# Optimization experiments

Hardware: AMD Instinct MI355X
Metric: run time of the kernel (lower is better)

The kernel has to match this reference:

```python
import jax, jax.numpy as jnp
import numpy as np

# Config constants (match init_kwargs)
THR = 0.2
TEMPERATURE = 0.1
BORDER_RM = 2
H0C, W0C = 60, 80  # L = 4800
H1C, W1C = 60, 80  # S = 4800


def setup_inputs() -> dict:
    key = jax.random.key(0)
    k0, k1 = jax.random.split(key)
    feat_c0 = jax.random.normal(k0, (2, 4800, 256), dtype=jnp.float32)
    feat_c1 = jax.random.normal(k1, (2, 4800, 256), dtype=jnp.float32)
    return {"feat_c0": feat_c0, "feat_c1": feat_c1}


def _border_mask_1d(h, w, b):
    """Flattened [h*w] bool mask that is False within b of any border."""
    ih = jnp.arange(h)
    iw = jnp.arange(w)
    mh = (ih >= b) & (ih < h - b)
    mw = (iw >= b) & (iw < w - b)
    return (mh[:, None] & mw[None, :]).reshape(-1)


def reference(feat_c0, feat_c1):
    N, L, C = feat_c0.shape
    # Normalize features and compute similarity (dual-softmax)
    scale = 1.0 / (C ** 0.5)
    sim = jnp.einsum('nlc,nsc->nls', feat_c0 * scale, feat_c1 * scale) / TEMPERATURE
    conf = jax.nn.softmax(sim, axis=1) * jax.nn.softmax(sim, axis=2)  # [N, L, S]

    # Threshold + border removal (mask_border path, no padding masks)
    bm0 = _border_mask_1d(H0C, W0C, BORDER_RM)  # [L]
    bm1 = _border_mask_1d(H1C, W1C, BORDER_RM)  # [S]
    mask = (conf > THR) & bm0[None, :, None] & bm1[None, None, :]

    # Mutual nearest neighbor
    mask = mask \
        & (conf == jnp.max(conf, axis=2, keepdims=True)) \
        & (conf == jnp.max(conf, axis=1, keepdims=True))

    # Per-row match: j index of the (at most one) surviving entry, and its conf.
    # Fixed-shape analogue of torch.where extraction: mconf==0 means no match.
    mask_v = jnp.any(mask, axis=2)                         # [N, L]
    j_ids = jnp.argmax(mask, axis=2)                       # [N, L]
    mconf = jnp.take_along_axis(conf, j_ids[..., None], axis=2)[..., 0]
    mconf = jnp.where(mask_v, mconf, 0.0)                  # [N, L]

    return conf, mask_v, j_ids, mconf
```

## Files before the change

### kernel.cpp

```cpp
#include <hip/hip_runtime.h>
#include <hip/hip_bf16.h>
#include <cstdint>

#define L_DIM 4800
#define C_DIM 256
#define CONF_ELEMS ((size_t)2 * L_DIM * L_DIM)

typedef _Float16 f16x8 __attribute__((ext_vector_type(8)));
typedef float f32x4 __attribute__((ext_vector_type(4)));

typedef const __attribute__((address_space(1))) uint32_t glb_u32;
typedef __attribute__((address_space(3))) uint32_t lds_u32;

#define WS_F16_NEEDED 15705600

__global__ __launch_bounds__(256) void k_cvt2(const float* __restrict__ f0,
                                              const float* __restrict__ f1,
                                              _Float16* __restrict__ h0,
                                              _Float16* __restrict__ h1) {
    int b = blockIdx.x;
    const float* src = (b < 1200) ? f0 : f1;
    _Float16* dst = (b < 1200) ? h0 : h1;
    int i = (b < 1200 ? b : b - 1200) * 256 + threadIdx.x;
    const float4* s4 = (const float4*)src;
    float4 a = s4[(size_t)i * 2], c = s4[(size_t)i * 2 + 1];
    f16x8 h = { (_Float16)a.x, (_Float16)a.y, (_Float16)a.z, (_Float16)a.w,
                (_Float16)c.x, (_Float16)c.y, (_Float16)c.z, (_Float16)c.w };
    *(f16x8*)(dst + (size_t)i * 8) = h;
}

__global__ __launch_bounds__(256) void k_reduceA(const float* __restrict__ partA,
                                                 float* __restrict__ invsum) {
    int i = blockIdx.x * 256 + threadIdx.x;
    if (i >= 19200) return;
    int base = (i < 9600) ? 0 : 50;
    int j = (i < 9600) ? i : i - 9600;
    float s = 0.f;
#pragma unroll 10
    for (int k = 0; k < 50; ++k)
        s += partA[(size_t)(base + k) * 9600 + j];
    invsum[i] = 1.0f / s;
}

template<bool F16SRC, bool FINAL>
__global__ __launch_bounds__(256) void k_gemm2(const void* __restrict__ srcA,
                                               const void* __restrict__ srcB,
                                               float* __restrict__ conf,
                                               const float* __restrict__ invsum,
                                               float* __restrict__ partA,
                                               unsigned long long* __restrict__ rowbest,
                                               unsigned* __restrict__ colbest) {
    const int xcd = blockIdx.x & 7;
    const int idx = blockIdx.x >> 3;
    const int t   = xcd * 625 + idx;
    const int n   = t / 2500;
    const int rem = t - n * 2500;
    const int ty  = rem / 50;
    const int tx  = rem - ty * 50;
    const int l0  = ty * 96;
    const int s0  = tx * 96;

    __shared__ __align__(16) _Float16 As[96 * 64];
    __shared__ __align__(16) _Float16 Bs[96 * 64];
    __shared__ __align__(16) char redbuf[2304];

    const int tid  = threadIdx.x;
    const int lane = tid & 63;
    const int w    = tid >> 6;
    const int wr   = w >> 1, wc = w & 1;
    const int q    = lane >> 4, r16 = lane & 15;

    f32x4 acc[3][3] = {};

    const _Float16* Ah = (const _Float16*)srcA + ((size_t)n * L_DIM + l0) * C_DIM;
    const _Float16* Bh = (const _Float16*)srcB + ((size_t)n * L_DIM + s0) * C_DIM;
    const float*    Af = (const float*)srcA + ((size_t)n * L_DIM + l0) * C_DIM;
    const float*    Bf = (const float*)srcB + ((size_t)n * L_DIM + s0) * C_DIM;

    for (int kt = 0; kt < 4; ++kt) {
        const int k0 = kt * 64;
        __syncthreads();
        if constexpr (F16SRC) {
#pragma unroll
            for (int i = 0; i < 3; ++i) {
                int c   = tid + i * 256;
                int row = c >> 3;
                int kc  = (c & 7) ^ (row & 7);
                __builtin_amdgcn_global_load_lds(
                    (glb_u32*)(Ah + (size_t)row * C_DIM + k0 + kc * 8),
                    (lds_u32*)(As + (i * 256 + w * 64) * 8), 16, 0, 0);
                __builtin_amdgcn_global_load_lds(
                    (glb_u32*)(Bh + (size_t)row * C_DIM + k0 + kc * 8),
                    (lds_u32*)(Bs + (i * 256 + w * 64) * 8), 16, 0, 0);
            }
        } else {
#pragma unroll
            for (int i = 0; i < 3; ++i) {
                int c   = tid + i * 256;
                int row = c >> 3;
                int kc  = (c & 7) ^ (row & 7);
                const float* pa = Af + (size_t)row * C_DIM + k0 + kc * 8;
                const float* pb = Bf + (size_t)row * C_DIM + k0 + kc * 8;
                float4 a0 = ((const float4*)pa)[0], a1 = ((const float4*)pa)[1];
                float4 b0 = ((const float4*)pb)[0], b1 = ((const float4*)pb)[1];
                f16x8 ha = { (_Float16)a0.x, (_Float16)a0.y, (_Float16)a0.z, (_Float16)a0.w,
                             (_Float16)a1.x, (_Float16)a1.y, (_Float16)a1.z, (_Float16)a1.w };
                f16x8 hb = { (_Float16)b0.x, (_Float16)b0.y, (_Float16)b0.z, (_Float16)b0.w,
                             (_Float16)b1.x, (_Float16)b1.y, (_Float16)b1.z, (_Float16)b1.w };
                *(f16x8*)(As + (size_t)c * 8) = ha;
                *(f16x8*)(Bs + (size_t)c * 8) = hb;
            }
        }
        __syncthreads();

        f16x8 af[2][3], bf[2][3];
#pragma unroll
        for (int m = 0; m < 3; ++m) {
            int row = wr * 48 + m * 16 + r16;
#pragma unroll
            for (int ks = 0; ks < 2; ++ks)
                af[ks][m] = *(const f16x8*)(As + row * 64 + (((ks * 4 + q) ^ (row & 7)) * 8));
        }
#pragma unroll
        for (int nn = 0; nn < 3; ++nn) {
            int row = wc * 48 + nn * 16 + r16;
#pragma unroll
            for (int ks = 0; ks < 2; ++ks)
                bf[ks][nn] = *(const f16x8*)(Bs + row * 64 + (((ks * 4 + q) ^ (row & 7)) * 8));
        }
#pragma unroll
        for (int ks = 0; ks < 2; ++ks)
#pragma unroll
            for (int m = 0; m < 3; ++m)
#pragma unroll
                for (int nn = 0; nn < 3; ++nn)
                    acc[m][nn] = __builtin_amdgcn_mfma_f32_16x16x32_f16(af[ks][m], bf[ks][nn], acc[m][nn], 0, 0, 0);
    }

    const float SIM_SCALE = 0.0390625f;

    if constexpr (!FINAL) {
        float* redR = (float*)redbuf;
        float* redC = (float*)(redbuf + 768);
        float cp[3] = {0.f, 0.f, 0.f};
#pragma unroll
        for (int m = 0; m < 3; ++m) {
#pragma unroll
            for (int reg = 0; reg < 4; ++reg) {
                float rsum = 0.f;
#pragma unroll
                for (int nn = 0; nn < 3; ++nn) {
                    float e = __expf(acc[m][nn][reg] * SIM_SCALE);
                    rsum += e;
                    cp[nn] += e;
                }
                rsum += __shfl_xor(rsum, 1);
                rsum += __shfl_xor(rsum, 2);
                rsum += __shfl_xor(rsum, 4);
                rsum += __shfl_xor(rsum, 8);
                if (r16 == 0)
                    redR[wc * 96 + wr * 48 + m * 16 + q * 4 + reg] = rsum;
            }
        }
#pragma unroll
        for (int nn = 0; nn < 3; ++nn) {
            float v = cp[nn];
            v += __shfl_xor(v, 16);
            v += __shfl_xor(v, 32);
            if (q == 0)
                redC[wr * 96 + wc * 48 + nn * 16 + r16] = v;
        }
        __syncthreads();
        if (tid < 96) {
            partA[(size_t)tx * 9600 + n * L_DIM + l0 + tid] = redR[tid] + redR[96 + tid];
        } else if (tid < 192) {
            int c = tid - 96;
            partA[(size_t)(50 + ty) * 9600 + n * L_DIM + s0 + c] = redC[c] + redC[96 + c];
        }
    } else {
        unsigned long long* redRB = (unsigned long long*)redbuf;
        unsigned* redCB = (unsigned*)(redbuf + 1536);
        const size_t base = (size_t)n * L_DIM * L_DIM;
        float ivC[3];
#pragma unroll
        for (int nn = 0; nn < 3; ++nn)
            ivC[nn] = invsum[9600 + n * L_DIM + s0 + wc * 48 + nn * 16 + r16];
        float cmx[3] = {0.f, 0.f, 0.f};
#pragma unroll
        for (int m = 0; m < 3; ++m) {
#pragma unroll
            for (int reg = 0; reg < 4; ++reg) {
                const int grow = l0 + wr * 48 + m * 16 + q * 4 + reg;
                const float ivR = invsum[n * L_DIM + grow];
                const size_t rowoff = base + (size_t)grow * L_DIM;
                float bv = -1.f; int bc = 0;
#pragma unroll
                for (int nn = 0; nn < 3; ++nn) {
                    const int gcol = s0 + wc * 48 + nn * 16 + r16;
                    float cf = __expf(acc[m][nn][reg] * (2.0f * SIM_SCALE)) * ivR * ivC[nn];
                    __builtin_nontemporal_store(cf, &conf[rowoff + gcol]);
                    cmx[nn] = fmaxf(cmx[nn], cf);
                    if (cf > bv) { bv = cf; bc = gcol; }
                }
                unsigned long long pack =
                    ((unsigned long long)__float_as_uint(bv) << 32) |
                    (unsigned long long)(0xFFFFFFFFu - (unsigned)bc);
#pragma unroll
                for (int d = 1; d < 16; d <<= 1) {
                    unsigned long long o = __shfl_xor(pack, d);
                    if (o > pack) pack = o;
                }
                if (r16 == 0)
                    redRB[wc * 96 + wr * 48 + m * 16 + q * 4 + reg] = pack;
            }
        }
#pragma unroll
        for (int nn = 0; nn < 3; ++nn) {
            float v = cmx[nn];
            v = fmaxf(v, __shfl_xor(v, 16));
            v = fmaxf(v, __shfl_xor(v, 32));
            if (q == 0)
                redCB[wr * 96 + wc * 48 + nn * 16 + r16] = __float_as_uint(v);
        }
        __syncthreads();
        if (tid < 96) {
            unsigned long long p0 = redRB[tid], p1 = redRB[96 + tid];
            rowbest[(size_t)tx * 9600 + n * L_DIM + l0 + tid] = (p0 > p1) ? p0 : p1;
        } else if (tid < 192) {
            int c = tid - 96;
            colbest[(size_t)ty * 9600 + n * L_DIM + s0 + c] = max(redCB[c], redCB[96 + c]);
        }
    }
}

__global__ __launch_bounds__(256) void k_match(const unsigned long long* __restrict__ rowbest,
                                               const unsigned* __restrict__ colbest,
                                               float* __restrict__ out) {
    int i = blockIdx.x * 256 + threadIdx.x;
    if (i >= 2 * L_DIM) return;
    unsigned long long p = 0ull;
#pragma unroll 10
    for (int k = 0; k < 50; ++k) {
        unsigned long long o = rowbest[(size_t)k * 9600 + i];
        if (o > p) p = o;
    }
    int n = i / L_DIM, l = i % L_DIM;
    float v = __uint_as_float((unsigned)(p >> 32));
    int cand = (int)(0xFFFFFFFFu - (unsigned)(p & 0xFFFFFFFFull));
    if (cand < 0 || cand >= L_DIM) cand = 0;
    unsigned cmu = 0u;
#pragma unroll 10
    for (int k = 0; k < 50; ++k)
        cmu = max(cmu, colbest[(size_t)k * 9600 + n * L_DIM + cand]);
    int h0 = l / 80, w0 = l % 80;
    int h1 = cand / 80, w1 = cand % 80;
    bool bm0 = (h0 >= 2) && (h0 < 58) && (w0 >= 2) && (w0 < 78);
    bool bm1 = (h1 >= 2) && (h1 < 58) && (w1 >= 2) && (w1 < 78);
    float cm = __uint_as_float(cmu);
    bool mask = (v > 0.2f) && bm0 && bm1 && (v == cm);
    out[CONF_ELEMS + i]         = mask ? 1.0f : 0.0f;
    out[CONF_ELEMS + 9600 + i]  = mask ? (float)cand : 0.0f;
    out[CONF_ELEMS + 19200 + i] = mask ? v : 0.0f;
}

extern "C" void kernel_launch(void* const* d_in, const int* in_sizes, int n_in,
                              void* d_out, int out_size, void* d_ws, size_t ws_size,
                              hipStream_t stream) {
    const float* f0 = (const float*)d_in[0];
    const float* f1 = (const float*)d_in[1];
    float* out = (float*)d_out;

    float* invsum = (float*)d_ws;
    float* partA = (float*)((char*)d_ws + 115200);
    unsigned long long* rowbest = (unsigned long long*)((char*)d_ws + 115200);
    unsigned* colbest = (unsigned*)((char*)d_ws + 3955200);
    _Float16* h0 = (_Float16*)((char*)d_ws + 5875200);
    _Float16* h1 = h0 + (size_t)2 * L_DIM * C_DIM;

    const bool usef16 = ws_size >= WS_F16_NEEDED;

    if (usef16) {
        k_cvt2<<<dim3(2400), 256, 0, stream>>>(f0, f1, h0, h1);
        k_gemm2<true, false><<<dim3(5000), 256, 0, stream>>>(
            h0, h1, out, invsum, partA, rowbest, colbest);
        k_reduceA<<<dim3(75), 256, 0, stream>>>(partA, invsum);
        k_gemm2<true, true><<<dim3(5000), 256, 0, stream>>>(
            h0, h1, out, invsum, partA, rowbest, colbest);
    } else {
        k_gemm2<false, false><<<dim3(5000), 256, 0, stream>>>(
            f0, f1, out, invsum, partA, rowbest, colbest);
        k_reduceA<<<dim3(75), 256, 0, stream>>>(partA, invsum);
        k_gemm2<false, true><<<dim3(5000), 256, 0, stream>>>(
            f0, f1, out, invsum, partA, rowbest, colbest);
    }
    k_match<<<dim3(38), 256, 0, stream>>>(rowbest, colbest, out);
}
```

Baseline: 135.5 us.

## Give each wave private LDS tiles to drop block-wide barriers in GEMM loop

New measurement: 161.4 us. 1.19x slower.

```diff
diff --git a/kernel.cpp b/kernel.cpp
--- a/kernel.cpp
+++ b/kernel.cpp
@@ -60,8 +60,7 @@
     const int l0  = ty * 96;
     const int s0  = tx * 96;
 
-    __shared__ __align__(16) _Float16 As[96 * 64];
-    __shared__ __align__(16) _Float16 Bs[96 * 64];
+    __shared__ __align__(16) _Float16 Sg[4 * 2 * 48 * 64];
     __shared__ __align__(16) char redbuf[2304];
 
     const int tid  = threadIdx.x;
@@ -70,35 +69,41 @@
     const int wr   = w >> 1, wc = w & 1;
     const int q    = lane >> 4, r16 = lane & 15;
 
+    _Float16* myA = Sg + w * 6144;
+    _Float16* myB = myA + 3072;
+
     f32x4 acc[3][3] = {};
 
-    const _Float16* Ah = (const _Float16*)srcA + ((size_t)n * L_DIM + l0) * C_DIM;
-    const _Float16* Bh = (const _Float16*)srcB + ((size_t)n * L_DIM + s0) * C_DIM;
-    const float*    Af = (const float*)srcA + ((size_t)n * L_DIM + l0) * C_DIM;
-    const float*    Bf = (const float*)srcB + ((size_t)n * L_DIM + s0) * C_DIM;
+    const _Float16* Ah = (const _Float16*)srcA + ((size_t)n * L_DIM + l0 + wr * 48) * C_DIM;
+    const _Float16* Bh = (const _Float16*)srcB + ((size_t)n * L_DIM + s0 + wc * 48) * C_DIM;
+    const float*    Af = (const float*)srcA + ((size_t)n * L_DIM + l0 + wr * 48) * C_DIM;
+    const float*    Bf = (const float*)srcB + ((size_t)n * L_DIM + s0 + wc * 48) * C_DIM;
 
     for (int kt = 0; kt < 4; ++kt) {
         const int k0 = kt * 64;
-        __syncthreads();
+        asm volatile("s_waitcnt lgkmcnt(0)" ::: "memory");
+        __builtin_amdgcn_sched_barrier(0);
         if constexpr (F16SRC) {
 #pragma unroll
-            for (int i = 0; i < 3; ++i) {
-                int c   = tid + i * 256;
-                int row = c >> 3;
-                int kc  = (c & 7) ^ (row & 7);
+            for (int jj = 0; jj < 6; ++jj) {
+                int c2  = lane + jj * 64;
+                int row = c2 >> 3;
+                int kc  = (c2 & 7) ^ (row & 7);
                 __builtin_amdgcn_global_load_lds(
                     (glb_u32*)(Ah + (size_t)row * C_DIM + k0 + kc * 8),
-                    (lds_u32*)(As + (i * 256 + w * 64) * 8), 16, 0, 0);
+                    (lds_u32*)(myA + jj * 64 * 8), 16, 0, 0);
                 __builtin_amdgcn_global_load_lds(
                     (glb_u32*)(Bh + (size_t)row * C_DIM + k0 + kc * 8),
-                    (lds_u32*)(Bs + (i * 256 + w * 64) * 8), 16, 0, 0);
+                    (lds_u32*)(myB + jj * 64 * 8), 16, 0, 0);
             }
+            asm volatile("s_waitcnt vmcnt(0)" ::: "memory");
+            __builtin_amdgcn_sched_barrier(0);
         } else {
 #pragma unroll
-            for (int i = 0; i < 3; ++i) {
-                int c   = tid + i * 256;
-                int row = c >> 3;
-                int kc  = (c & 7) ^ (row & 7);
+            for (int jj = 0; jj < 6; ++jj) {
+                int c2  = lane + jj * 64;
+                int row = c2 >> 3;
+                int kc  = (c2 & 7) ^ (row & 7);
                 const float* pa = Af + (size_t)row * C_DIM + k0 + kc * 8;
                 const float* pb = Bf + (size_t)row * C_DIM + k0 + kc * 8;
                 float4 a0 = ((const float4*)pa)[0], a1 = ((const float4*)pa)[1];
@@ -107,26 +112,27 @@
                              (_Float16)a1.x, (_Float16)a1.y, (_Float16)a1.z, (_Float16)a1.w };
                 f16x8 hb = { (_Float16)b0.x, (_Float16)b0.y, (_Float16)b0.z, (_Float16)b0.w,
                              (_Float16)b1.x, (_Float16)b1.y, (_Float16)b1.z, (_Float16)b1.w };
-                *(f16x8*)(As + (size_t)c * 8) = ha;
-                *(f16x8*)(Bs + (size_t)c * 8) = hb;
+                *(f16x8*)(myA + c2 * 8) = ha;
+                *(f16x8*)(myB + c2 * 8) = hb;
             }
-        }
-        __syncthreads();
+            asm volatile("s_waitcnt lgkmcnt(0)" ::: "memory");
+            __builtin_amdgcn_sched_barrier(0);
+        }
 
         f16x8 af[2][3], bf[2][3];
 #pragma unroll
         for (int m = 0; m < 3; ++m) {
-            int row = wr * 48 + m * 16 + r16;
+            int r = m * 16 + r16;
 #pragma unroll
             for (int ks = 0; ks < 2; ++ks)
-                af[ks][m] = *(const f16x8*)(As + row * 64 + (((ks * 4 + q) ^ (row & 7)) * 8));
+                af[ks][m] = *(const f16x8*)(myA + r * 64 + (((ks * 4 + q) ^ (r & 7)) * 8));
         }
 #pragma unroll
         for (int nn = 0; nn < 3; ++nn) {
-            int row = wc * 48 + nn * 16 + r16;
+            int r = nn * 16 + r16;
 #pragma unroll
             for (int ks = 0; ks < 2; ++ks)
-                bf[ks][nn] = *(const f16x8*)(Bs + row * 64 + (((ks * 4 + q) ^ (row & 7)) * 8));
+                bf[ks][nn] = *(const f16x8*)(myB + r * 64 + (((ks * 4 + q) ^ (r & 7)) * 8));
         }
 #pragma unroll
         for (int ks = 0; ks < 2; ++ks)
```
